# Optimization experiments

Hardware: AMD Instinct MI355X
Metric: run time of the kernel (lower is better)

The kernel has to match this reference:

```python
import jax, jax.numpy as jnp
import numpy as np

N_HEADS = 12   # hard-coded in Attention.__init__
HEAD_DIM = 64  # hard-coded in Attention.__init__


def setup_inputs() -> dict:
    key = jax.random.key(0)
    ks = jax.random.split(key, 6)
    S, B, D = 512, 8, 1024
    NB = 8
    BD = D // NB                 # 128
    E = N_HEADS * HEAD_DIM       # 768
    sc = 0.02
    return {
        'x':       jax.random.normal(ks[0], (S, B, D), jnp.float32),
        'w_comp':  jax.random.normal(ks[1], (NB, BD, 1), jnp.float32) * 0.05,
        'wq':      jax.random.normal(ks[2], (NB, BD, E), jnp.float32) * sc,
        'wk':      jax.random.normal(ks[3], (NB, BD, E), jnp.float32) * sc,
        'wv':      jax.random.normal(ks[4], (NB, BD, E), jnp.float32) * sc,
        'w_final': jax.random.normal(ks[5], (NB, E, BD), jnp.float32) * sc,
    }


def reference(x, w_comp, wq, wk, wv, w_final):
    S, B, D = x.shape
    NB, BD, E = wq.shape
    nh, hd = N_HEADS, HEAD_DIM
    scale = hd ** (-0.5)

    xb = x.reshape(S, B, NB, BD)  # split into blocks

    # competition-based block gating: GroupLinear(block_dim -> 1) + softmax over blocks
    comp_logits = jnp.einsum('sbnd,ndo->sbno', xb, w_comp)[..., 0]  # [S,B,NB]
    comp = jax.nn.softmax(comp_logits, axis=2)
    xg = xb * comp[..., None]

    # block-wise GroupLinear QKV projections -> [S,B,NB,nh,hd]
    q = jnp.einsum('sbnd,nde->sbne', xg, wq).reshape(S, B, NB, nh, hd)
    k = jnp.einsum('sbnd,nde->sbne', xg, wk).reshape(S, B, NB, nh, hd)
    v = jnp.einsum('sbnd,nde->sbne', xg, wv).reshape(S, B, NB, nh, hd)

    # transpose(2,3): heads before blocks -> attention over the block axis
    q = jnp.swapaxes(q, 2, 3) * scale  # [S,B,nh,NB,hd]
    k = jnp.swapaxes(k, 2, 3)
    v = jnp.swapaxes(v, 2, 3)

    score = jnp.einsum('sbhnd,sbhmd->sbhnm', q, k)  # [S,B,nh,NB,NB]
    attn = jax.nn.softmax(score, axis=-1)
    out = jnp.einsum('sbhnm,sbhmd->sbhnd', attn, v)  # [S,B,nh,NB,hd]

    out = jnp.swapaxes(out, 2, 3).reshape(S, B, NB, nh * hd)
    out = jnp.einsum('sbne,ned->sbnd', out, w_final).reshape(S, B, D)

    score_mean = attn.mean(axis=2)  # mean over heads -> [S,B,NB,NB]
    return out, score_mean
```

## Files before the change

### kernel.cpp

```cpp
#include <hip/hip_runtime.h>
#include <hip/hip_bf16.h>

typedef __bf16 bf16;
typedef __bf16 bf16x8 __attribute__((ext_vector_type(8)));
typedef float f32x4 __attribute__((ext_vector_type(4)));

#define S_TOK 4096
#define D_DIM 1024
#define NBLK 8
#define BDIM 128
#define E_DIM 768
#define NH 12
#define HD 64
#define QKVW 2304
#define PADW 2312

__global__ __launch_bounds__(256) void prep_weights(
    const float* __restrict__ wq, const float* __restrict__ wk,
    const float* __restrict__ wv, const float* __restrict__ wfin,
    bf16* __restrict__ wcatT, bf16* __restrict__ wfinT) {
  long idx = (long)blockIdx.x * 256 + threadIdx.x;
  const long NCAT = (long)NBLK * QKVW * BDIM;
  if (idx < NCAT) {
    int k = idx & (BDIM - 1);
    long rem = idx >> 7;
    int j = (int)(rem % QKVW);
    int n = (int)(rem / QKVW);
    const float* src; int jj;
    if (j < 768) { src = wq; jj = j; }
    else if (j < 1536) { src = wk; jj = j - 768; }
    else { src = wv; jj = j - 1536; }
    float v = src[((long)n * BDIM + k) * E_DIM + jj];
    wcatT[idx] = (bf16)v;
  } else {
    long i2 = idx - NCAT;
    if (i2 < (long)NBLK * BDIM * E_DIM) {
      int e = (int)(i2 % E_DIM);
      long rem = i2 / E_DIM;
      int d = (int)(rem & (BDIM - 1));
      int n = (int)(rem >> 7);
      float v = wfin[((long)n * E_DIM + e) * BDIM + d];
      wfinT[i2] = (bf16)v;
    }
  }
}

__global__ __launch_bounds__(256) void gate_kernel(
    const float* __restrict__ x, const float* __restrict__ wcomp,
    bf16* __restrict__ xg) {
  int tok = blockIdx.x;
  int t = threadIdx.x;
  int n = t >> 5;
  int l = t & 31;
  const float* xrow = x + (long)tok * D_DIM + n * BDIM;
  float xv[4]; float part = 0.f;
#pragma unroll
  for (int i = 0; i < 4; ++i) {
    int d = l + i * 32;
    xv[i] = xrow[d];
    part += xv[i] * wcomp[n * BDIM + d];
  }
#pragma unroll
  for (int m = 16; m >= 1; m >>= 1) part += __shfl_xor(part, m, 64);
  __shared__ float logits[NBLK];
  __shared__ float comp[NBLK];
  if (l == 0) logits[n] = part;
  __syncthreads();
  if (t == 0) {
    float mx = logits[0];
#pragma unroll
    for (int i = 1; i < 8; ++i) mx = fmaxf(mx, logits[i]);
    float s = 0.f, e[8];
#pragma unroll
    for (int i = 0; i < 8; ++i) { e[i] = __expf(logits[i] - mx); s += e[i]; }
    float inv = 1.f / s;
#pragma unroll
    for (int i = 0; i < 8; ++i) comp[i] = e[i] * inv;
  }
  __syncthreads();
  float c = comp[n];
  bf16* dst = xg + ((long)n * S_TOK + tok) * BDIM;
#pragma unroll
  for (int i = 0; i < 4; ++i) dst[l + i * 32] = (bf16)(xv[i] * c);
}

__device__ __forceinline__ void stage_tile(char* lds, const char* g, long rstride) {
  int wave = threadIdx.x >> 6, lane = threadIdx.x & 63;
#pragma unroll
  for (int s = 0; s < 8; ++s) {
    int instr = wave * 8 + s;
    int row = instr * 4 + (lane >> 4);
    int chunk = (lane & 15) ^ (row & 7);
    const char* src = g + (long)row * rstride + chunk * 16;
    __builtin_amdgcn_global_load_lds(
        (const __attribute__((address_space(1))) void*)src,
        (__attribute__((address_space(3))) void*)(lds + instr * 1024), 16, 0, 0);
  }
}

__device__ __forceinline__ bf16x8 ld_frag(const char* lds, int row, int kchunk) {
  int chunk = kchunk ^ (row & 7);
  return *(const bf16x8*)(lds + row * 256 + chunk * 16);
}

__device__ __forceinline__ void mfma_slab(const char* ldsA, const char* ldsB,
                                          f32x4 acc[4][4], int wm, int wn, int lane) {
#pragma unroll
  for (int ks = 0; ks < 4; ++ks) {
    int kchunk = ks * 4 + (lane >> 4);
    bf16x8 af[4], bfr[4];
#pragma unroll
    for (int i = 0; i < 4; ++i) af[i] = ld_frag(ldsA, wm + i * 16 + (lane & 15), kchunk);
#pragma unroll
    for (int j = 0; j < 4; ++j) bfr[j] = ld_frag(ldsB, wn + j * 16 + (lane & 15), kchunk);
#pragma unroll
    for (int i = 0; i < 4; ++i)
#pragma unroll
      for (int j = 0; j < 4; ++j)
        acc[i][j] = __builtin_amdgcn_mfma_f32_16x16x32_bf16(af[i], bfr[j], acc[i][j], 0, 0, 0);
  }
}

__global__ __launch_bounds__(256) void qkv_gemm(
    const bf16* __restrict__ xg, const bf16* __restrict__ wcatT,
    bf16* __restrict__ qkv, int t0) {
  __shared__ char ldsA[32768];
  __shared__ char ldsB[32768];
  int nt = blockIdx.x;
  int mt = blockIdx.y;
  int blk = blockIdx.z;
  const char* Ab = (const char*)(xg + ((long)blk * S_TOK + t0 + mt * 128) * BDIM);
  const char* Bb = (const char*)(wcatT + ((long)blk * QKVW + nt * 128) * BDIM);
  stage_tile(ldsA, Ab, 256);
  stage_tile(ldsB, Bb, 256);
  __syncthreads();
  int wave = threadIdx.x >> 6, lane = threadIdx.x & 63;
  int wm = (wave >> 1) * 64, wn = (wave & 1) * 64;
  f32x4 acc[4][4] = {};
  mfma_slab(ldsA, ldsB, acc, wm, wn, lane);
  int rbase = (lane >> 4) * 4;
  int cb = lane & 15;
  long tokl0 = (long)mt * 128;
#pragma unroll
  for (int i = 0; i < 4; ++i) {
#pragma unroll
    for (int r = 0; r < 4; ++r) {
      long tokl = tokl0 + wm + i * 16 + rbase + r;
      bf16* dst = qkv + tokl * (NBLK * QKVW) + (long)blk * QKVW + nt * 128 + wn + cb;
#pragma unroll
      for (int j = 0; j < 4; ++j) dst[j * 16] = (bf16)acc[i][j][r];
    }
  }
}

__global__ __launch_bounds__(256) void attn_kernel(
    const bf16* __restrict__ qkv, bf16* __restrict__ attn_out,
    float* __restrict__ out2, int t0, int TC) {
  __shared__ short qlds[NBLK * PADW];
  __shared__ float smp[4][64];
  int tl = blockIdx.x;
  long tok = t0 + tl;
  int t = threadIdx.x;
  const uint4* src = (const uint4*)(qkv + (long)tl * NBLK * QKVW);
#pragma unroll
  for (int i = 0; i < 9; ++i) {
    int c = t + i * 256;
    int n = c / 288;
    int w = c - n * 288;
    *(uint4*)(&qlds[n * PADW + w * 8]) = src[c];
  }
  __syncthreads();
  int wave = t >> 6, lane = t & 63;
  int n = lane >> 3, mo = lane & 7;
  const bf16* lds = (const bf16*)qlds;
  float smacc = 0.f;
#pragma unroll
  for (int hi = 0; hi < 3; ++hi) {
    int h = wave + hi * 4;
    float s = 0.f;
#pragma unroll
    for (int dd = 0; dd < 8; ++dd) {
      bf16x8 q8 = *(const bf16x8*)(lds + n * PADW + h * HD + dd * 8);
      bf16x8 k8 = *(const bf16x8*)(lds + mo * PADW + 768 + h * HD + dd * 8);
#pragma unroll
      for (int u = 0; u < 8; ++u) s += (float)q8[u] * (float)k8[u];
    }
    s *= 0.125f;
    float mx = s;
#pragma unroll
    for (int msk = 1; msk < 8; msk <<= 1) mx = fmaxf(mx, __shfl_xor(mx, msk, 64));
    float p = __expf(s - mx);
    float sum = p;
#pragma unroll
    for (int msk = 1; msk < 8; msk <<= 1) sum += __shfl_xor(sum, msk, 64);
    float a = p / sum;
    smacc += a;
    float o[8] = {};
#pragma unroll
    for (int m = 0; m < 8; ++m) {
      float am = __shfl(a, (lane & 56) | m, 64);
      bf16x8 v8 = *(const bf16x8*)(lds + m * PADW + 1536 + h * HD + mo * 8);
#pragma unroll
      for (int u = 0; u < 8; ++u) o[u] += am * (float)v8[u];
    }
    bf16x8 ov;
#pragma unroll
    for (int u = 0; u < 8; ++u) ov[u] = (bf16)o[u];
    *(bf16x8*)(attn_out + ((long)n * TC + tl) * E_DIM + h * HD + mo * 8) = ov;
  }
  smp[wave][lane] = smacc;
  __syncthreads();
  if (t < 64) {
    float v = (smp[0][t] + smp[1][t] + smp[2][t] + smp[3][t]) * (1.f / 12.f);
    out2[tok * 64 + t] = v;
  }
}

__global__ __launch_bounds__(256) void final_gemm(
    const bf16* __restrict__ attn_out, const bf16* __restrict__ wfinT,
    float* __restrict__ out, int t0, int TC) {
  __shared__ char ldsA[32768];
  __shared__ char ldsB[32768];
  int mt = blockIdx.y;
  int blk = blockIdx.z;
  int wave = threadIdx.x >> 6, lane = threadIdx.x & 63;
  int wm = (wave >> 1) * 64, wn = (wave & 1) * 64;
  f32x4 acc[4][4] = {};
  const char* Abase = (const char*)(attn_out + ((long)blk * TC + mt * 128) * E_DIM);
  const char* Bbase = (const char*)(wfinT + (long)blk * BDIM * E_DIM);
  for (int kt = 0; kt < 6; ++kt) {
    stage_tile(ldsA, Abase + kt * 256, E_DIM * 2);
    stage_tile(ldsB, Bbase + kt * 256, E_DIM * 2);
    __syncthreads();
    mfma_slab(ldsA, ldsB, acc, wm, wn, lane);
    __syncthreads();
  }
  int rbase = (lane >> 4) * 4;
  int cb = lane & 15;
#pragma unroll
  for (int i = 0; i < 4; ++i) {
#pragma unroll
    for (int r = 0; r < 4; ++r) {
      long tok = (long)t0 + mt * 128 + wm + i * 16 + rbase + r;
      float* dst = out + tok * D_DIM + blk * BDIM + wn + cb;
#pragma unroll
      for (int j = 0; j < 4; ++j) dst[j * 16] = acc[i][j][r];
    }
  }
}

extern "C" void kernel_launch(void* const* d_in, const int* in_sizes, int n_in,
                              void* d_out, int out_size, void* d_ws, size_t ws_size,
                              hipStream_t stream) {
  const float* x     = (const float*)d_in[0];
  const float* wcomp = (const float*)d_in[1];
  const float* wq    = (const float*)d_in[2];
  const float* wk    = (const float*)d_in[3];
  const float* wv    = (const float*)d_in[4];
  const float* wfin  = (const float*)d_in[5];
  float* out  = (float*)d_out;
  float* out2 = out + (long)S_TOK * D_DIM;

  char* ws = (char*)d_ws;
  bf16* xg    = (bf16*)ws;
  bf16* wcatT = (bf16*)(ws + 8388608);
  bf16* wfinT = (bf16*)(ws + 8388608 + 4718592);
  char* dyn   = ws + 14680064;
  long TC = (long)((ws_size > 14680064 ? ws_size - 14680064 : 0) / 49152);
  if (TC > S_TOK) TC = S_TOK;
  TC &= ~127L;
  if (TC < 128) TC = 128;
  bf16* qkvb  = (bf16*)dyn;
  bf16* attnb = (bf16*)(dyn + TC * 36864L);

  prep_weights<<<12288, 256, 0, stream>>>(wq, wk, wv, wfin, wcatT, wfinT);
  gate_kernel<<<S_TOK, 256, 0, stream>>>(x, wcomp, xg);
  for (int t0 = 0; t0 < S_TOK; t0 += (int)TC) {
    int tc = S_TOK - t0; if (tc > TC) tc = (int)TC;
    dim3 g2(18, tc / 128, 8);
    qkv_gemm<<<g2, 256, 0, stream>>>(xg, wcatT, qkvb, t0);
    attn_kernel<<<tc, 256, 0, stream>>>(qkvb, attnb, out2, t0, tc);
    dim3 g4(1, tc / 128, 8);
    final_gemm<<<g4, 256, 0, stream>>>(attnb, wfinT, out, t0, tc);
  }
}
```

Baseline: 196.4 us.

## Replace LDS staging in attention with register shuffles; run final GEMM once

The attention kernel no longer stages the per-token QKV tile into LDS. Each lane loads its own q/k/v 16-byte chunk from global memory and exchanges k and v vectors across lanes with wave shuffles, computing all 8 scores per lane. The attention output buffer now holds the full token range, so the final GEMM runs as one launch over all tokens instead of once per chunk. This removes the LDS round trip and a barrier per block plus per-chunk launch overhead, at the cost of many more shuffles and a fixed 48 MB workspace reservation that shrinks the QKV chunk size.

After: 220.9 us. +12.5%, slower.

```diff
diff --git a/kernel.cpp b/kernel.cpp
--- a/kernel.cpp
+++ b/kernel.cpp
@@ -13,7 +13,6 @@
 #define NH 12
 #define HD 64
 #define QKVW 2304
-#define PADW 2312
 
 __global__ __launch_bounds__(256) void prep_weights(
     const float* __restrict__ wq, const float* __restrict__ wk,
@@ -153,62 +152,76 @@
   }
 }
 
+__device__ __forceinline__ int4 shfl4(int4 v, int src) {
+  int4 r;
+  r.x = __shfl(v.x, src, 64); r.y = __shfl(v.y, src, 64);
+  r.z = __shfl(v.z, src, 64); r.w = __shfl(v.w, src, 64);
+  return r;
+}
+
 __global__ __launch_bounds__(256) void attn_kernel(
     const bf16* __restrict__ qkv, bf16* __restrict__ attn_out,
-    float* __restrict__ out2, int t0, int TC) {
-  __shared__ short qlds[NBLK * PADW];
+    float* __restrict__ out2, int t0) {
   __shared__ float smp[4][64];
+  int t = threadIdx.x;
+  int wave = t >> 6, lane = t & 63;
   int tl = blockIdx.x;
   long tok = t0 + tl;
-  int t = threadIdx.x;
-  const uint4* src = (const uint4*)(qkv + (long)tl * NBLK * QKVW);
-#pragma unroll
-  for (int i = 0; i < 9; ++i) {
-    int c = t + i * 256;
-    int n = c / 288;
-    int w = c - n * 288;
-    *(uint4*)(&qlds[n * PADW + w * 8]) = src[c];
-  }
-  __syncthreads();
-  int wave = t >> 6, lane = t & 63;
-  int n = lane >> 3, mo = lane & 7;
-  const bf16* lds = (const bf16*)qlds;
-  float smacc = 0.f;
+  int n = lane >> 3, c = lane & 7;
+  const bf16* base = qkv + (long)tl * (NBLK * QKVW) + n * QKVW + c * 8;
+  float smacc[8] = {};
 #pragma unroll
   for (int hi = 0; hi < 3; ++hi) {
     int h = wave + hi * 4;
-    float s = 0.f;
-#pragma unroll
-    for (int dd = 0; dd < 8; ++dd) {
-      bf16x8 q8 = *(const bf16x8*)(lds + n * PADW + h * HD + dd * 8);
-      bf16x8 k8 = *(const bf16x8*)(lds + mo * PADW + 768 + h * HD + dd * 8);
-#pragma unroll
-      for (int u = 0; u < 8; ++u) s += (float)q8[u] * (float)k8[u];
-    }
-    s *= 0.125f;
-    float mx = s;
-#pragma unroll
-    for (int msk = 1; msk < 8; msk <<= 1) mx = fmaxf(mx, __shfl_xor(mx, msk, 64));
-    float p = __expf(s - mx);
-    float sum = p;
-#pragma unroll
-    for (int msk = 1; msk < 8; msk <<= 1) sum += __shfl_xor(sum, msk, 64);
-    float a = p / sum;
-    smacc += a;
-    float o[8] = {};
+    const bf16* hb = base + h * HD;
+    int4 q4 = *(const int4*)(hb);
+    int4 k4 = *(const int4*)(hb + E_DIM);
+    int4 v4 = *(const int4*)(hb + 2 * E_DIM);
+    bf16x8 q8 = __builtin_bit_cast(bf16x8, q4);
+    float qf[8];
+#pragma unroll
+    for (int u = 0; u < 8; ++u) qf[u] = (float)q8[u];
+    float sp[8];
 #pragma unroll
     for (int m = 0; m < 8; ++m) {
-      float am = __shfl(a, (lane & 56) | m, 64);
-      bf16x8 v8 = *(const bf16x8*)(lds + m * PADW + 1536 + h * HD + mo * 8);
-#pragma unroll
-      for (int u = 0; u < 8; ++u) o[u] += am * (float)v8[u];
+      bf16x8 km = __builtin_bit_cast(bf16x8, shfl4(k4, m * 8 + c));
+      float acc = 0.f;
+#pragma unroll
+      for (int u = 0; u < 8; ++u) acc += qf[u] * (float)km[u];
+      sp[m] = acc;
+    }
+#pragma unroll
+    for (int m = 0; m < 8; ++m) {
+#pragma unroll
+      for (int msk = 1; msk < 8; msk <<= 1) sp[m] += __shfl_xor(sp[m], msk, 64);
+      sp[m] *= 0.125f;
+    }
+    float mx = sp[0];
+#pragma unroll
+    for (int m = 1; m < 8; ++m) mx = fmaxf(mx, sp[m]);
+    float a[8]; float ssum = 0.f;
+#pragma unroll
+    for (int m = 0; m < 8; ++m) { a[m] = __expf(sp[m] - mx); ssum += a[m]; }
+    float inv = 1.f / ssum;
+#pragma unroll
+    for (int m = 0; m < 8; ++m) { a[m] *= inv; smacc[m] += a[m]; }
+    float of[8] = {};
+#pragma unroll
+    for (int m = 0; m < 8; ++m) {
+      bf16x8 vm = __builtin_bit_cast(bf16x8, shfl4(v4, m * 8 + c));
+#pragma unroll
+      for (int u = 0; u < 8; ++u) of[u] += a[m] * (float)vm[u];
     }
     bf16x8 ov;
 #pragma unroll
-    for (int u = 0; u < 8; ++u) ov[u] = (bf16)o[u];
-    *(bf16x8*)(attn_out + ((long)n * TC + tl) * E_DIM + h * HD + mo * 8) = ov;
-  }
-  smp[wave][lane] = smacc;
+    for (int u = 0; u < 8; ++u) ov[u] = (bf16)of[u];
+    *(int4*)(attn_out + ((long)n * S_TOK + tok) * E_DIM + h * HD + c * 8) =
+        __builtin_bit_cast(int4, ov);
+  }
+  float sel = smacc[0];
+#pragma unroll
+  for (int m = 1; m < 8; ++m) if (c == m) sel = smacc[m];
+  smp[wave][lane] = sel;
   __syncthreads();
   if (t < 64) {
     float v = (smp[0][t] + smp[1][t] + smp[2][t] + smp[3][t]) * (1.f / 12.f);
@@ -218,7 +231,7 @@
 
 __global__ __launch_bounds__(256) void final_gemm(
     const bf16* __restrict__ attn_out, const bf16* __restrict__ wfinT,
-    float* __restrict__ out, int t0, int TC) {
+    float* __restrict__ out) {
   __shared__ char ldsA[32768];
   __shared__ char ldsB[32768];
   int mt = blockIdx.y;
@@ -226,7 +239,7 @@
   int wave = threadIdx.x >> 6, lane = threadIdx.x & 63;
   int wm = (wave >> 1) * 64, wn = (wave & 1) * 64;
   f32x4 acc[4][4] = {};
-  const char* Abase = (const char*)(attn_out + ((long)blk * TC + mt * 128) * E_DIM);
+  const char* Abase = (const char*)(attn_out + ((long)blk * S_TOK + mt * 128) * E_DIM);
   const char* Bbase = (const char*)(wfinT + (long)blk * BDIM * E_DIM);
   for (int kt = 0; kt < 6; ++kt) {
     stage_tile(ldsA, Abase + kt * 256, E_DIM * 2);
@@ -241,7 +254,7 @@
   for (int i = 0; i < 4; ++i) {
 #pragma unroll
     for (int r = 0; r < 4; ++r) {
-      long tok = (long)t0 + mt * 128 + wm + i * 16 + rbase + r;
+      long tok = (long)mt * 128 + wm + i * 16 + rbase + r;
       float* dst = out + tok * D_DIM + blk * BDIM + wn + cb;
 #pragma unroll
       for (int j = 0; j < 4; ++j) dst[j * 16] = acc[i][j][r];
@@ -265,13 +278,16 @@
   bf16* xg    = (bf16*)ws;
   bf16* wcatT = (bf16*)(ws + 8388608);
   bf16* wfinT = (bf16*)(ws + 8388608 + 4718592);
-  char* dyn   = ws + 14680064;
-  long TC = (long)((ws_size > 14680064 ? ws_size - 14680064 : 0) / 49152);
-  if (TC > S_TOK) TC = S_TOK;
+  const long FIXED = 14680064;
+  bf16* attnb = (bf16*)(ws + FIXED);
+  const long ATTNB = 50331648;
+  char* dyn = ws + FIXED + ATTNB;
+  long avail = (long)ws_size - (FIXED + ATTNB);
+  long TC = avail > 0 ? avail / 36864 : 0;
+  if (TC > 2048) TC = 2048;
   TC &= ~127L;
   if (TC < 128) TC = 128;
-  bf16* qkvb  = (bf16*)dyn;
-  bf16* attnb = (bf16*)(dyn + TC * 36864L);
+  bf16* qkvb = (bf16*)dyn;
 
   prep_weights<<<12288, 256, 0, stream>>>(wq, wk, wv, wfin, wcatT, wfinT);
   gate_kernel<<<S_TOK, 256, 0, stream>>>(x, wcomp, xg);
@@ -279,8 +295,8 @@
     int tc = S_TOK - t0; if (tc > TC) tc = (int)TC;
     dim3 g2(18, tc / 128, 8);
     qkv_gemm<<<g2, 256, 0, stream>>>(xg, wcatT, qkvb, t0);
-    attn_kernel<<<tc, 256, 0, stream>>>(qkvb, attnb, out2, t0, tc);
-    dim3 g4(1, tc / 128, 8);
-    final_gemm<<<g4, 256, 0, stream>>>(attnb, wfinT, out, t0, tc);
-  }
-}
+    attn_kernel<<<tc, 256, 0, stream>>>(qkvb, attnb, out2, t0);
+  }
+  dim3 g4(1, 32, 8);
+  final_gemm<<<g4, 256, 0, stream>>>(attnb, wfinT, out);
+}
```
